# Performance work log

Hardware: AMD Instinct MI355X
Metric: run time of the kernel (lower is better)

The kernel has to match this reference:

```python
import jax, jax.numpy as jnp
import numpy as np

EPS = 1e-12  # torch F.normalize default eps

def _l2_normalize(x):
    # F.normalize(x, dim=1): x / max(||x||_2, eps), per row
    n = jnp.linalg.norm(x, axis=1, keepdims=True)
    return x / jnp.maximum(n, EPS)

def setup_inputs() -> dict:
    key = jax.random.key(0)
    ks = jax.random.split(key, 7)
    B, D = 8192, 4096
    s = 1.0 / np.sqrt(D)  # keep activations well-scaled like nn.Linear init
    return {
        "x":  jax.random.normal(ks[0], (B, D), dtype=jnp.float32),
        "W0": jax.random.normal(ks[1], (D, D), dtype=jnp.float32) * s,
        "b0": jax.random.normal(ks[2], (D,),   dtype=jnp.float32) * s,
        "W1": jax.random.normal(ks[3], (D, D), dtype=jnp.float32) * s,
        "b1": jax.random.normal(ks[4], (D,),   dtype=jnp.float32) * s,
        "W2": jax.random.normal(ks[5], (D, D), dtype=jnp.float32) * s,
        "b2": jax.random.normal(ks[6], (D,),   dtype=jnp.float32) * s,
    }

def reference(x, W0, b0, W1, b1, W2, b2):
    # per layer: out = relu(Linear(l2_normalize(x, dim=1))); collect all layer outputs
    params = [(W0, b0), (W1, b1), (W2, b2)]
    outs = []
    h = x
    for W, b in params:
        hn = _l2_normalize(h)
        # nn.Linear stores weight as [out, in]: y = hn @ W.T + b
        h = jax.nn.relu(jnp.einsum('bi,oi->bo', hn, W) + b)
        outs.append(h)
    return tuple(outs)
```

## Files before the change

kernel.cpp:

```cpp
#include <hip/hip_runtime.h>
#include <hip/hip_bf16.h>


#define NROWS 8192
#define DIM   4096

typedef __bf16 bf16x8 __attribute__((ext_vector_type(8)));
typedef float  f32x4  __attribute__((ext_vector_type(4)));

__device__ static inline short f2bf(float f) {
  __hip_bfloat16 h = __float2bfloat16(f);
  return __builtin_bit_cast(short, h);
}

#define BARRIER() do { asm volatile("" ::: "memory"); \
                       __builtin_amdgcn_s_barrier();  \
                       asm volatile("" ::: "memory"); } while (0)
#define LGKM0()  asm volatile("s_waitcnt lgkmcnt(0)" ::: "memory")

__global__ __launch_bounds__(512, 2)
void gemm256_bias_relu(const short* __restrict__ A,
                       const short* __restrict__ Bw,
                       const float* __restrict__ bias,
                       float* __restrict__ C,
                       int M, int N, int K)
{
  __shared__ short lds[4][16384];

  int bid = blockIdx.x;
  const int nwg = gridDim.x;
  if ((nwg & 7) == 0) { const int cpx = nwg >> 3; bid = (bid & 7) * cpx + (bid >> 3); }
  const int nbn  = N >> 8;
  const int brow = (bid / nbn) << 8;
  const int bcol = (bid % nbn) << 8;

  const int lane = threadIdx.x & 63;
  const int wid  = threadIdx.x >> 6;
  const int wr   = wid >> 2;
  const int wc   = wid & 3;

  float bv[4];
#pragma unroll
  for (int j = 0; j < 4; ++j)
    bv[j] = bias[bcol + wc * 64 + j * 16 + (lane & 15)];

  f32x4 acc[8][4] = {};

  const size_t Kz   = (size_t)K;
  const size_t rowK = Kz * 2;
  char* const  ldsB = (char*)&lds[0][0];

  const int r8  = lane >> 3;
  const int kcs = (lane & 7) ^ r8;
  const char* AgL = (const char*)A  + (size_t)(brow + r8) * rowK + (size_t)kcs * 16;
  const char* BgL = (const char*)Bw + (size_t)(bcol + r8) * rowK + (size_t)kcs * 16;
  size_t rbo[4];
  int    rbb[4];
#pragma unroll
  for (int i = 0; i < 4; ++i) {
    const int rb = wid * 8 + i * 64;
    rbo[i] = (size_t)rb * rowK;
    rbb[i] = rb * 128;
  }

  auto stage_half = [&](int parity, int op, int h, int tile) {
    const char* gp = (op ? BgL : AgL) + ((size_t)tile << 7);
    char* lb = ldsB + (parity * 2 + op) * 32768;
#pragma unroll
    for (int s = 0; s < 2; ++s) {
      const int idx = h * 2 + s;
      __builtin_amdgcn_global_load_lds(
          (const __attribute__((address_space(1))) void*)(gp + rbo[idx]),
          (__attribute__((address_space(3))) void*)(lb + rbb[idx]), 16, 0, 0);
    }
  };

  const int l15  = lane & 15;
  const int xlo  = ((lane >> 4) ^ (lane & 3)) * 16;
  const int b2   = (lane >> 2) & 1;
  const int k64[2] = { b2 << 6, (1 - b2) << 6 };
  const int abase = (wr * 128 + l15) * 128 + xlo;
  const int bbase = (wc * 64  + l15) * 128 + xlo;

  const int NT = K >> 6;

  bf16x8 aS[2][2][2];
  bf16x8 bF[4][2];

#define LOAD_A(SET, I0, PTR)                                                 \
  _Pragma("unroll")                                                          \
  for (int ii = 0; ii < 2; ++ii)                                             \
    _Pragma("unroll")                                                        \
    for (int ks = 0; ks < 2; ++ks)                                           \
      aS[SET][ii][ks] = *reinterpret_cast<const bf16x8*>(                    \
          (PTR) + abase + ((I0) + ii) * 2048 + k64[ks]);

#define MFMA2(I0, SET)                                                       \
  _Pragma("unroll")                                                          \
  for (int ks = 0; ks < 2; ++ks)                                             \
    _Pragma("unroll")                                                        \
    for (int ii = 0; ii < 2; ++ii)                                           \
      _Pragma("unroll")                                                      \
      for (int j = 0; j < 4; ++j)                                            \
        acc[(I0) + ii][j] = __builtin_amdgcn_mfma_f32_16x16x32_bf16(         \
            aS[SET][ii][ks], bF[j][ks], acc[(I0) + ii][j], 0, 0, 0);

  stage_half(0, 0, 0, 0); stage_half(0, 0, 1, 0);
  stage_half(0, 1, 0, 0); stage_half(0, 1, 1, 0);
  if (NT > 1) { stage_half(1, 1, 0, 1); stage_half(1, 1, 1, 1); }
  if (NT > 1) asm volatile("s_waitcnt vmcnt(4)" ::: "memory");
  else        asm volatile("s_waitcnt vmcnt(0)" ::: "memory");
  BARRIER();
  {
    const char* A0 = ldsB;
    LOAD_A(0, 0, A0)
  }

  for (int t = 0; t < NT; ++t) {
    const int cur = t & 1, nxt = cur ^ 1;
    const char* At = ldsB + (cur * 2 + 0) * 32768;
    const char* Bt = ldsB + (cur * 2 + 1) * 32768;
    const char* An = ldsB + (nxt * 2 + 0) * 32768;

    if (t + 1 < NT) stage_half(nxt, 0, 0, t + 1);
#pragma unroll
    for (int j = 0; j < 4; ++j)
#pragma unroll
      for (int ks = 0; ks < 2; ++ks)
        bF[j][ks] = *reinterpret_cast<const bf16x8*>(Bt + bbase + j * 2048 + k64[ks]);
    BARRIER();
    LGKM0();
    LOAD_A(1, 2, At)
    __builtin_amdgcn_s_setprio(1);
    MFMA2(0, 0)
    __builtin_amdgcn_s_setprio(0);

    if (t + 1 < NT) stage_half(nxt, 0, 1, t + 1);
    BARRIER();
    LGKM0();
    LOAD_A(0, 4, At)
    __builtin_amdgcn_s_setprio(1);
    MFMA2(2, 1)
    __builtin_amdgcn_s_setprio(0);

    if (t + 2 < NT) stage_half(cur, 1, 0, t + 2);
    LOAD_A(1, 6, At)
    BARRIER();
    LGKM0();
    __builtin_amdgcn_s_setprio(1);
    MFMA2(4, 0)
    __builtin_amdgcn_s_setprio(0);

    if (t + 2 < NT) stage_half(cur, 1, 1, t + 2);
    if (t >= NT - 2) asm volatile("s_waitcnt vmcnt(0)" ::: "memory");
    else             asm volatile("s_waitcnt vmcnt(4)" ::: "memory");
    BARRIER();
    LGKM0();
    if (t + 1 < NT) { LOAD_A(0, 0, An) }
    __builtin_amdgcn_s_setprio(1);
    MFMA2(6, 1)
    __builtin_amdgcn_s_setprio(0);
  }
#undef MFMA2
#undef LOAD_A

#pragma unroll
  for (int i = 0; i < 8; ++i) {
    const int rbase = brow + wr * 128 + i * 16 + ((lane >> 4) << 2);
#pragma unroll
    for (int j = 0; j < 4; ++j) {
      const int col = bcol + wc * 64 + j * 16 + (lane & 15);
#pragma unroll
      for (int r = 0; r < 4; ++r) {
        const float v = acc[i][j][r] + bv[j];
        C[(size_t)(rbase + r) * N + col] = v > 0.f ? v : 0.f;
      }
    }
  }
}

__global__ __launch_bounds__(256)
void rownorm_bf16(const float* __restrict__ in, short* __restrict__ out)
{
  const int row = blockIdx.x;
  const int t0  = threadIdx.x;
  const float4* inr = (const float4*)(in + (size_t)row * DIM);

  float4 v[4];
  float ss = 0.f;
#pragma unroll
  for (int t = 0; t < 4; ++t) {
    v[t] = inr[t0 + t * 256];
    ss += v[t].x * v[t].x + v[t].y * v[t].y + v[t].z * v[t].z + v[t].w * v[t].w;
  }
#pragma unroll
  for (int off = 32; off > 0; off >>= 1)
    ss += __shfl_down(ss, off, 64);

  __shared__ float wss[4];
  if ((t0 & 63) == 0) wss[t0 >> 6] = ss;
  __syncthreads();
  const float tot   = wss[0] + wss[1] + wss[2] + wss[3];
  const float scale = 1.f / fmaxf(sqrtf(tot), 1e-12f);

  short4* outr = (short4*)(out + (size_t)row * DIM);
#pragma unroll
  for (int t = 0; t < 4; ++t) {
    short4 o;
    o.x = f2bf(v[t].x * scale);
    o.y = f2bf(v[t].y * scale);
    o.z = f2bf(v[t].z * scale);
    o.w = f2bf(v[t].w * scale);
    outr[t0 + t * 256] = o;
  }
}

__global__ __launch_bounds__(256)
void cast_bf16(const float* __restrict__ in, short* __restrict__ out, int n4)
{
  int i = blockIdx.x * 256 + threadIdx.x;
  const int stride = gridDim.x * 256;
  for (; i < n4; i += stride) {
    const float4 v = ((const float4*)in)[i];
    short4 o;
    o.x = f2bf(v.x);
    o.y = f2bf(v.y);
    o.z = f2bf(v.z);
    o.w = f2bf(v.w);
    ((short4*)out)[i] = o;
  }
}

extern "C" void kernel_launch(void* const* d_in, const int* in_sizes, int n_in,
                              void* d_out, int out_size, void* d_ws, size_t ws_size,
                              hipStream_t stream) {
  const float* x = (const float*)d_in[0];
  const float* W[3]    = { (const float*)d_in[1], (const float*)d_in[3], (const float*)d_in[5] };
  const float* bias[3] = { (const float*)d_in[2], (const float*)d_in[4], (const float*)d_in[6] };
  float* out = (float*)d_out;

  short* hn = (short*)d_ws;
  short* Wb = (short*)((char*)d_ws + (size_t)NROWS * DIM * 2);

  const size_t layer_elems = (size_t)NROWS * DIM;
  const float* hin = x;

  for (int L = 0; L < 3; ++L) {
    cast_bf16<<<2048, 256, 0, stream>>>(W[L], Wb, DIM * DIM / 4);
    rownorm_bf16<<<NROWS, 256, 0, stream>>>(hin, hn);
    gemm256_bias_relu<<<(NROWS / 256) * (DIM / 256), 512, 0, stream>>>(
        hn, Wb, bias[L], out + (size_t)L * layer_elems, NROWS, DIM, DIM);
    hin = out + (size_t)L * layer_elems;
  }
}
```

Before: 797.9 us.

## Restructure GEMM main loop into two phases with larger A fragment batches

The GEMM inner loop drops from four barrier-separated phases to two. Each phase now loads four A row-fragments and issues 32 MFMAs, and the next tile's global-to-LDS stages are issued as whole tiles rather than halves. A sched_barrier after each lgkmcnt wait pins the instruction order. The wave id is made scalar with readfirstlane and the row offsets become 32-bit, which cuts address arithmetic. The aim is fewer barriers and larger MFMA bursts per sync, at the cost of more VGPRs for fragments and a full vmcnt(0) drain each iteration that may expose global load latency.

```diff
diff --git a/kernel.cpp b/kernel.cpp
--- a/kernel.cpp
+++ b/kernel.cpp
@@ -16,7 +16,8 @@
 #define BARRIER() do { asm volatile("" ::: "memory"); \
                        __builtin_amdgcn_s_barrier();  \
                        asm volatile("" ::: "memory"); } while (0)
-#define LGKM0()  asm volatile("s_waitcnt lgkmcnt(0)" ::: "memory")
+#define GATE()   do { asm volatile("s_waitcnt lgkmcnt(0)" ::: "memory"); \
+                      __builtin_amdgcn_sched_barrier(0); } while (0)
 
 __global__ __launch_bounds__(512, 2)
 void gemm256_bias_relu(const short* __restrict__ A,
@@ -35,7 +36,7 @@
   const int bcol = (bid % nbn) << 8;
 
   const int lane = threadIdx.x & 63;
-  const int wid  = threadIdx.x >> 6;
+  const int wid  = __builtin_amdgcn_readfirstlane(threadIdx.x >> 6);
   const int wr   = wid >> 2;
   const int wc   = wid & 3;
 
@@ -46,20 +47,18 @@
 
   f32x4 acc[8][4] = {};
 
-  const size_t Kz   = (size_t)K;
-  const size_t rowK = Kz * 2;
+  const size_t rowK = (size_t)K * 2;
   char* const  ldsB = (char*)&lds[0][0];
 
   const int r8  = lane >> 3;
   const int kcs = (lane & 7) ^ r8;
   const char* AgL = (const char*)A  + (size_t)(brow + r8) * rowK + (size_t)kcs * 16;
   const char* BgL = (const char*)Bw + (size_t)(bcol + r8) * rowK + (size_t)kcs * 16;
-  size_t rbo[4];
-  int    rbb[4];
+  int rbo[4], rbb[4];
 #pragma unroll
   for (int i = 0; i < 4; ++i) {
     const int rb = wid * 8 + i * 64;
-    rbo[i] = (size_t)rb * rowK;
+    rbo[i] = rb * (int)rowK;
     rbb[i] = rb * 128;
   }
 
@@ -84,26 +83,25 @@
 
   const int NT = K >> 6;
 
-  bf16x8 aS[2][2][2];
-  bf16x8 bF[4][2];
-
-#define LOAD_A(SET, I0, PTR)                                                 \
+  bf16x8 aX[4][2], aY[4][2], bF[4][2];
+
+#define LOAD_FRAG(DST, PTR, BASE, I0)                                        \
   _Pragma("unroll")                                                          \
-  for (int ii = 0; ii < 2; ++ii)                                             \
+  for (int ii = 0; ii < 4; ++ii)                                             \
     _Pragma("unroll")                                                        \
     for (int ks = 0; ks < 2; ++ks)                                           \
-      aS[SET][ii][ks] = *reinterpret_cast<const bf16x8*>(                    \
-          (PTR) + abase + ((I0) + ii) * 2048 + k64[ks]);
-
-#define MFMA2(I0, SET)                                                       \
+      DST[ii][ks] = *reinterpret_cast<const bf16x8*>(                        \
+          (PTR) + (BASE) + ((I0) + ii) * 2048 + k64[ks]);
+
+#define MFMA16(I0, AF)                                                       \
   _Pragma("unroll")                                                          \
   for (int ks = 0; ks < 2; ++ks)                                             \
     _Pragma("unroll")                                                        \
-    for (int ii = 0; ii < 2; ++ii)                                           \
+    for (int ii = 0; ii < 4; ++ii)                                           \
       _Pragma("unroll")                                                      \
       for (int j = 0; j < 4; ++j)                                            \
         acc[(I0) + ii][j] = __builtin_amdgcn_mfma_f32_16x16x32_bf16(         \
-            aS[SET][ii][ks], bF[j][ks], acc[(I0) + ii][j], 0, 0, 0);
+            AF[ii][ks], bF[j][ks], acc[(I0) + ii][j], 0, 0, 0);
 
   stage_half(0, 0, 0, 0); stage_half(0, 0, 1, 0);
   stage_half(0, 1, 0, 0); stage_half(0, 1, 1, 0);
@@ -111,10 +109,7 @@
   if (NT > 1) asm volatile("s_waitcnt vmcnt(4)" ::: "memory");
   else        asm volatile("s_waitcnt vmcnt(0)" ::: "memory");
   BARRIER();
-  {
-    const char* A0 = ldsB;
-    LOAD_A(0, 0, A0)
-  }
+  LOAD_FRAG(aX, ldsB, abase, 0)
 
   for (int t = 0; t < NT; ++t) {
     const int cur = t & 1, nxt = cur ^ 1;
@@ -122,47 +117,26 @@
     const char* Bt = ldsB + (cur * 2 + 1) * 32768;
     const char* An = ldsB + (nxt * 2 + 0) * 32768;
 
-    if (t + 1 < NT) stage_half(nxt, 0, 0, t + 1);
-#pragma unroll
-    for (int j = 0; j < 4; ++j)
-#pragma unroll
-      for (int ks = 0; ks < 2; ++ks)
-        bF[j][ks] = *reinterpret_cast<const bf16x8*>(Bt + bbase + j * 2048 + k64[ks]);
+    if (t + 1 < NT) { stage_half(nxt, 0, 0, t + 1); stage_half(nxt, 0, 1, t + 1); }
+    LOAD_FRAG(bF, Bt, bbase, 0)
     BARRIER();
-    LGKM0();
-    LOAD_A(1, 2, At)
+    GATE();
+    LOAD_FRAG(aY, At, abase, 4)
     __builtin_amdgcn_s_setprio(1);
-    MFMA2(0, 0)
+    MFMA16(0, aX)
     __builtin_amdgcn_s_setprio(0);
 
-    if (t + 1 < NT) stage_half(nxt, 0, 1, t + 1);
+    asm volatile("s_waitcnt vmcnt(0)" ::: "memory");
     BARRIER();
-    LGKM0();
-    LOAD_A(0, 4, At)
+    GATE();
+    if (t + 2 < NT) { stage_half(cur, 1, 0, t + 2); stage_half(cur, 1, 1, t + 2); }
+    if (t + 1 < NT) { LOAD_FRAG(aX, An, abase, 0) }
     __builtin_amdgcn_s_setprio(1);
-    MFMA2(2, 1)
+    MFMA16(4, aY)
     __builtin_amdgcn_s_setprio(0);
-
-    if (t + 2 < NT) stage_half(cur, 1, 0, t + 2);
-    LOAD_A(1, 6, At)
-    BARRIER();
-    LGKM0();
-    __builtin_amdgcn_s_setprio(1);
-    MFMA2(4, 0)
-    __builtin_amdgcn_s_setprio(0);
-
-    if (t + 2 < NT) stage_half(cur, 1, 1, t + 2);
-    if (t >= NT - 2) asm volatile("s_waitcnt vmcnt(0)" ::: "memory");
-    else             asm volatile("s_waitcnt vmcnt(4)" ::: "memory");
-    BARRIER();
-    LGKM0();
-    if (t + 1 < NT) { LOAD_A(0, 0, An) }
-    __builtin_amdgcn_s_setprio(1);
-    MFMA2(6, 1)
-    __builtin_amdgcn_s_setprio(0);
-  }
-#undef MFMA2
-#undef LOAD_A
+  }
+#undef MFMA16
+#undef LOAD_FRAG
 
 #pragma unroll
   for (int i = 0; i < 8; ++i) {
```

After: 779.2 us (median of 2 runs). -2.3%, faster.
